# Kernel tuning notes

Hardware: AMD Instinct MI355X
Metric: run time of the kernel (lower is better)

## Reference

```python
import jax, jax.numpy as jnp
import numpy as np

N_NODES = 50000
N_EDGES = 800000
IN_DIM, H1, H2, OUT_DIM = 128, 512, 256, 1


def glorot(key, shape):
    fan_in, fan_out = shape
    lim = jnp.sqrt(6.0 / (fan_in + fan_out))
    return jax.random.uniform(key, shape, jnp.float32, -lim, lim)


def setup_inputs() -> dict:
    key = jax.random.key(0)
    ks = jax.random.split(key, 6)
    x = jax.random.normal(ks[0], (N_NODES, IN_DIM), jnp.float32)
    edge_index = jax.random.randint(ks[1], (2, N_EDGES), 0, N_NODES, jnp.int32)
    edge_attr = jax.random.uniform(ks[2], (N_EDGES,), jnp.float32)
    return {
        "x": x,
        "edge_index": edge_index,
        "edge_attr": edge_attr,
        "W1": glorot(ks[3], (IN_DIM, H1)), "b1": jnp.zeros((H1,), jnp.float32),
        "W2": glorot(ks[4], (H1, H2)), "b2": jnp.zeros((H2,), jnp.float32),
        "W3": glorot(ks[5], (H2, OUT_DIM)), "b3": jnp.zeros((OUT_DIM,), jnp.float32),
    }


def gcn_conv(x, src, dst, ew, W, b, n_nodes):
    # PyG GCNConv with edge weights, normalize=True, add_self_loops=True.
    h = x @ W                                            # [N, F_out]
    # degree includes self-loop weight 1.0 at each node
    deg = jax.ops.segment_sum(ew, dst, num_segments=n_nodes) + 1.0  # [N]
    dis = jnp.where(deg > 0, jax.lax.rsqrt(deg), 0.0)    # deg^{-1/2}
    norm = dis[src] * ew * dis[dst]                      # [E]
    msgs = h[src] * norm[:, None]                        # [E, F_out] gather
    agg = jax.ops.segment_sum(msgs, dst, num_segments=n_nodes)      # scatter-add
    # self-loop contribution: norm_ii = dis_i * 1 * dis_i = 1/deg_i
    agg = agg + h * (dis * dis)[:, None]
    return agg + b


def reference(x, edge_index, edge_attr, W1, b1, W2, b2, W3, b3):
    src, dst = edge_index[0], edge_index[1]
    n = x.shape[0]
    h = jax.nn.relu(gcn_conv(x, src, dst, edge_attr, W1, b1, n))
    h = jax.nn.relu(gcn_conv(h, src, dst, edge_attr, W2, b2, n))
    return gcn_conv(h, src, dst, edge_attr, W3, b3, n)
```

## Files before the change

kernel.cpp:

```cpp
#include <hip/hip_runtime.h>
#include <hip/hip_bf16.h>
#include <stdint.h>

typedef unsigned short u16;
typedef unsigned long long u64;
typedef __attribute__((ext_vector_type(8))) short bf16x8;
typedef __attribute__((ext_vector_type(4))) float f32x4;

constexpr int N_NODES = 50000;
constexpr int N_EDGES = 800000;
constexpr int IN_DIM  = 128;
constexpr int H1_DIM  = 512;
constexpr int H2_DIM  = 256;
constexpr int MT      = 64;
constexpr int MP      = 50048;

constexpr float DEG_SCALE = 268435456.0f;
constexpr float DEG_INV   = 1.0f / 268435456.0f;

__device__ __forceinline__ u16 f2b(float f) {
  union { float f; unsigned u; } v{f};
  unsigned r = v.u + 0x7fff + ((v.u >> 16) & 1);
  return (u16)(r >> 16);
}
__device__ __forceinline__ float b2f(u16 h) {
  union { unsigned u; float f; } v;
  v.u = ((unsigned)h) << 16;
  return v.f;
}

__device__ __forceinline__ void async16(void* lds, const void* g) {
  __builtin_amdgcn_global_load_lds(
      (const __attribute__((address_space(1))) unsigned int*)g,
      (__attribute__((address_space(3))) unsigned int*)lds, 16, 0, 0);
}

__global__ __launch_bounds__(256) void deg_hist_kernel(
    const int* __restrict__ dst, const float* __restrict__ ew,
    u64* __restrict__ degcnt, int E) {
  int e = blockIdx.x * 256 + threadIdx.x;
  if (e >= E) return;
  int d = dst[e];
  u64 inc = ((u64)1 << 40) | (u64)(ew[e] * DEG_SCALE + 0.5f);
  atomicAdd(&degcnt[d], inc);
}

__global__ __launch_bounds__(256) void scan1_kernel(
    const u64* __restrict__ degcnt, int* __restrict__ counts,
    float* __restrict__ dis, int* __restrict__ row_ptr,
    int* __restrict__ bsum, int n) {
  __shared__ int ws[4];
  int b = blockIdx.x, t = threadIdx.x, idx = b * 256 + t;
  int lane = t & 63, wid = t >> 6;
  u64 v = (idx < n) ? degcnt[idx] : 0;
  int cnt = (int)(v >> 40);
  if (idx < n) {
    counts[idx] = cnt;
    float deg = (float)(v & 0xFFFFFFFFFFULL) * DEG_INV;
    dis[idx] = rsqrtf(deg + 1.0f);
  }
  int val = cnt;
#pragma unroll
  for (int off = 1; off < 64; off <<= 1) {
    int u = __shfl_up(val, off);
    if (lane >= off) val += u;
  }
  if (lane == 63) ws[wid] = val;
  __syncthreads();
  if (t == 0) {
    int s = 0;
#pragma unroll
    for (int j = 0; j < 4; ++j) { int q = ws[j]; ws[j] = s; s += q; }
    bsum[b] = s;
  }
  __syncthreads();
  val += ws[wid];
  if (idx < n) row_ptr[idx + 1] = val;
}

__global__ __launch_bounds__(256) void scan2_kernel(int* bsum, int nb) {
  __shared__ int ws[4];
  int t = threadIdx.x;
  int lane = t & 63, wid = t >> 6;
  int self = (t < nb) ? bsum[t] : 0;
  int val = self;
#pragma unroll
  for (int off = 1; off < 64; off <<= 1) {
    int u = __shfl_up(val, off);
    if (lane >= off) val += u;
  }
  if (lane == 63) ws[wid] = val;
  __syncthreads();
  if (t == 0) {
    int s = 0;
#pragma unroll
    for (int j = 0; j < 4; ++j) { int q = ws[j]; ws[j] = s; s += q; }
  }
  __syncthreads();
  val += ws[wid];
  if (t < nb) bsum[t] = val - self;
}

__global__ __launch_bounds__(256) void scan3_kernel(
    int* __restrict__ row_ptr, const int* __restrict__ bsum, int n) {
  int idx = blockIdx.x * 256 + threadIdx.x;
  if (idx < n) row_ptr[idx + 1] += bsum[blockIdx.x];
  if (idx == 0) row_ptr[0] = 0;
}

__global__ __launch_bounds__(256) void fill_kernel(
    const int* __restrict__ src, const int* __restrict__ dst,
    const float* __restrict__ ew, const float* __restrict__ dis,
    const int* __restrict__ row_ptr, int* __restrict__ counts,
    u64* __restrict__ erec, int E) {
  int e = blockIdx.x * 256 + threadIdx.x;
  if (e >= E) return;
  int d = dst[e], s = src[e];
  int pos = row_ptr[d] + atomicSub(&counts[d], 1) - 1;
  float nm = dis[s] * ew[e] * dis[d];
  erec[pos] = ((u64)__float_as_uint(nm) << 32) | (unsigned)s;
}

__global__ __launch_bounds__(256) void cvt_bf16_kernel(
    const float* __restrict__ in, u16* __restrict__ out, int n4) {
  int i = blockIdx.x * 256 + threadIdx.x;
  if (i >= n4) return;
  float4 v = *(const float4*)&in[(size_t)i * 4];
  ushort4 o;
  o.x = f2b(v.x); o.y = f2b(v.y); o.z = f2b(v.z); o.w = f2b(v.w);
  *(ushort4*)&out[(size_t)i * 4] = o;
}

__global__ __launch_bounds__(256) void agg128_kernel(
    const u16* __restrict__ X, const int* __restrict__ row_ptr,
    const u64* __restrict__ erec, const float* __restrict__ dis,
    u16* __restrict__ Y, int n) {
  int wid = threadIdx.x >> 6, lane = threadIdx.x & 63;
  int node = blockIdx.x * 4 + wid;
  if (node >= n) return;
  float d = dis[node];
  float dd = d * d;
  const u16* Xl = X + lane * 2;
  ushort2 sv = *(const ushort2*)(Xl + (size_t)node * 128);
  float a0 = b2f(sv.x) * dd, a1 = b2f(sv.y) * dd;
  int e0 = row_ptr[node], e1 = row_ptr[node + 1];
  for (int base = e0; base < e1; base += 64) {
    int cnt = min(64, e1 - base);
    u64 rec = 0;
    if (lane < cnt) rec = erec[base + lane];
    int sl = (int)(unsigned)rec;
    float wl = __uint_as_float((unsigned)(rec >> 32));
    int j = 0;
    for (; j + 4 <= cnt; j += 4) {
      int   s0 = __shfl(sl, j),     s1 = __shfl(sl, j + 1);
      int   s2 = __shfl(sl, j + 2), s3 = __shfl(sl, j + 3);
      float w0 = __shfl(wl, j),     w1 = __shfl(wl, j + 1);
      float w2 = __shfl(wl, j + 2), w3 = __shfl(wl, j + 3);
      ushort2 v0 = *(const ushort2*)(Xl + (size_t)s0 * 128);
      ushort2 v1 = *(const ushort2*)(Xl + (size_t)s1 * 128);
      ushort2 v2 = *(const ushort2*)(Xl + (size_t)s2 * 128);
      ushort2 v3 = *(const ushort2*)(Xl + (size_t)s3 * 128);
      a0 += b2f(v0.x) * w0; a1 += b2f(v0.y) * w0;
      a0 += b2f(v1.x) * w1; a1 += b2f(v1.y) * w1;
      a0 += b2f(v2.x) * w2; a1 += b2f(v2.y) * w2;
      a0 += b2f(v3.x) * w3; a1 += b2f(v3.y) * w3;
    }
    for (; j < cnt; ++j) {
      int s0 = __shfl(sl, j); float w0 = __shfl(wl, j);
      ushort2 v0 = *(const ushort2*)(Xl + (size_t)s0 * 128);
      a0 += b2f(v0.x) * w0; a1 += b2f(v0.y) * w0;
    }
  }
  unsigned pk = ((unsigned)f2b(a1) << 16) | (unsigned)f2b(a0);
  *(unsigned*)(Y + (size_t)node * 128 + lane * 2) = pk;
}

__global__ __launch_bounds__(256) void agg256_gemv_kernel(
    const u16* __restrict__ X, const int* __restrict__ row_ptr,
    const u64* __restrict__ erec, const float* __restrict__ dis,
    const float* __restrict__ b2, const float* __restrict__ W3,
    float* __restrict__ T, int n) {
  int wid = threadIdx.x >> 6, lane = threadIdx.x & 63;
  int node = blockIdx.x * 4 + wid;
  if (node >= n) return;
  float d = dis[node];
  float dd = d * d;
  const u16* Xl = X + lane * 4;
  ushort4 sv = *(const ushort4*)(Xl + (size_t)node * 256);
  float a0 = b2f(sv.x) * dd, a1 = b2f(sv.y) * dd;
  float a2 = b2f(sv.z) * dd, a3 = b2f(sv.w) * dd;
  int e0 = row_ptr[node], e1 = row_ptr[node + 1];
  for (int base = e0; base < e1; base += 64) {
    int cnt = min(64, e1 - base);
    u64 rec = 0;
    if (lane < cnt) rec = erec[base + lane];
    int sl = (int)(unsigned)rec;
    float wl = __uint_as_float((unsigned)(rec >> 32));
    int j = 0;
    for (; j + 4 <= cnt; j += 4) {
      int   s0 = __shfl(sl, j),     s1 = __shfl(sl, j + 1);
      int   s2 = __shfl(sl, j + 2), s3 = __shfl(sl, j + 3);
      float w0 = __shfl(wl, j),     w1 = __shfl(wl, j + 1);
      float w2 = __shfl(wl, j + 2), w3 = __shfl(wl, j + 3);
      ushort4 v0 = *(const ushort4*)(Xl + (size_t)s0 * 256);
      ushort4 v1 = *(const ushort4*)(Xl + (size_t)s1 * 256);
      ushort4 v2 = *(const ushort4*)(Xl + (size_t)s2 * 256);
      ushort4 v3 = *(const ushort4*)(Xl + (size_t)s3 * 256);
      a0 += b2f(v0.x) * w0; a1 += b2f(v0.y) * w0;
      a2 += b2f(v0.z) * w0; a3 += b2f(v0.w) * w0;
      a0 += b2f(v1.x) * w1; a1 += b2f(v1.y) * w1;
      a2 += b2f(v1.z) * w1; a3 += b2f(v1.w) * w1;
      a0 += b2f(v2.x) * w2; a1 += b2f(v2.y) * w2;
      a2 += b2f(v2.z) * w2; a3 += b2f(v2.w) * w2;
      a0 += b2f(v3.x) * w3; a1 += b2f(v3.y) * w3;
      a2 += b2f(v3.z) * w3; a3 += b2f(v3.w) * w3;
    }
    for (; j < cnt; ++j) {
      int s0 = __shfl(sl, j); float w0 = __shfl(wl, j);
      ushort4 v0 = *(const ushort4*)(Xl + (size_t)s0 * 256);
      a0 += b2f(v0.x) * w0; a1 += b2f(v0.y) * w0;
      a2 += b2f(v0.z) * w0; a3 += b2f(v0.w) * w0;
    }
  }
  float4 bv = *(const float4*)&b2[lane * 4];
  float4 wv = *(const float4*)&W3[lane * 4];
  float s = fmaxf(a0 + bv.x, 0.f) * wv.x + fmaxf(a1 + bv.y, 0.f) * wv.y +
            fmaxf(a2 + bv.z, 0.f) * wv.z + fmaxf(a3 + bv.w, 0.f) * wv.w;
#pragma unroll
  for (int off = 32; off; off >>= 1) s += __shfl_down(s, off);
  if (lane == 0) T[node] = s;
}

__global__ __launch_bounds__(256) void transpose_bf16_kernel(
    const float* __restrict__ W, u16* __restrict__ Wt, int K, int N) {
  int i = blockIdx.x * 256 + threadIdx.x;
  if (i >= N * K) return;
  int n = i / K, k = i - n * K;
  Wt[i] = f2b(W[(size_t)k * N + n]);
}

__global__ __launch_bounds__(512, 4) void fused_gemm_kernel(
    const u16* __restrict__ xa, const u16* __restrict__ w1t,
    const u16* __restrict__ w2t, const float* __restrict__ b1,
    u16* __restrict__ t2b, int Mstore) {
  __shared__ u16 xa_s[MT * 128];
  __shared__ u16 h1_s[MT * 128];
  __shared__ u16 ws_s[256 * 64];
  int tid = threadIdx.x;
  int m0 = blockIdx.x * MT;
  int lane = tid & 63, w = tid >> 6;
  int l15 = lane & 15, l4 = lane >> 4;
  int wa = w >> 1;
  int wb = w & 1;

  {
    const char* xb = (const char*)xa + (size_t)m0 * 256;
#pragma unroll
    for (int i = 0; i < 2; ++i) {
      int L = i * 8192 + tid * 16;
      int row = L >> 8;
      int srcoff = (row << 8) + ((L & 255) ^ ((row & 7) << 4));
      async16((char*)xa_s + i * 8192 + (tid & ~63) * 16, xb + srcoff);
    }
  }

  f32x4 acc2[4][2];
#pragma unroll
  for (int i = 0; i < 4; ++i)
#pragma unroll
    for (int j = 0; j < 2; ++j) acc2[i][j] = (f32x4){0.f, 0.f, 0.f, 0.f};

  for (int c = 0; c < 4; ++c) {
    f32x4 acc1[2][2];
#pragma unroll
    for (int i = 0; i < 2; ++i)
#pragma unroll
      for (int j = 0; j < 2; ++j) acc1[i][j] = (f32x4){0.f, 0.f, 0.f, 0.f};

#pragma unroll
    for (int ko = 0; ko < 2; ++ko) {
      {
        const char* wsrc = (const char*)w1t + (size_t)(c * 128) * 256 + ko * 128;
#pragma unroll
        for (int i = 0; i < 2; ++i) {
          int L = i * 8192 + tid * 16;
          int row = L >> 7;
          int srcoff = (row << 8) + ((L & 127) ^ ((row & 7) << 4));
          async16((char*)ws_s + i * 8192 + (tid & ~63) * 16, wsrc + srcoff);
        }
      }
      __syncthreads();
#pragma unroll
      for (int ki = 0; ki < 2; ++ki) {
        bf16x8 a1[2], bx[2];
#pragma unroll
        for (int fn = 0; fn < 2; ++fn) {
          int nr = wa * 32 + fn * 16 + l15;
          int byte = (nr * 128 + ki * 64 + l4 * 16) ^ ((nr & 7) << 4);
          a1[fn] = *(const bf16x8*)((const char*)ws_s + byte);
        }
#pragma unroll
        for (int fm = 0; fm < 2; ++fm) {
          int mr = wb * 32 + fm * 16 + l15;
          int byte = (mr * 256 + ko * 128 + ki * 64 + l4 * 16) ^ ((mr & 7) << 4);
          bx[fm] = *(const bf16x8*)((const char*)xa_s + byte);
        }
#pragma unroll
        for (int fn = 0; fn < 2; ++fn)
#pragma unroll
          for (int fm = 0; fm < 2; ++fm)
            acc1[fn][fm] = __builtin_amdgcn_mfma_f32_16x16x32_bf16(
                a1[fn], bx[fm], acc1[fn][fm], 0, 0, 0);
      }
      __syncthreads();
    }

#pragma unroll
    for (int fn = 0; fn < 2; ++fn) {
      int nloc = wa * 32 + fn * 16 + l4 * 4;
      float4 bv = *(const float4*)&b1[c * 128 + nloc];
#pragma unroll
      for (int fm = 0; fm < 2; ++fm) {
        int mr = wb * 32 + fm * 16 + l15;
        u16 p0 = f2b(fmaxf(acc1[fn][fm][0] + bv.x, 0.f));
        u16 p1 = f2b(fmaxf(acc1[fn][fm][1] + bv.y, 0.f));
        u16 p2 = f2b(fmaxf(acc1[fn][fm][2] + bv.z, 0.f));
        u16 p3 = f2b(fmaxf(acc1[fn][fm][3] + bv.w, 0.f));
        u64 pk = ((u64)p3 << 48) | ((u64)p2 << 32) | ((u64)p1 << 16) | p0;
        int byte = (mr * 256 + nloc * 2) ^ ((mr & 7) << 4);
        *(u64*)((char*)h1_s + byte) = pk;
      }
    }
    __syncthreads();

#pragma unroll
    for (int ko = 0; ko < 2; ++ko) {
      {
        const char* wsrc = (const char*)w2t + (size_t)(c * 128 + ko * 64) * 2;
#pragma unroll
        for (int i = 0; i < 4; ++i) {
          int L = i * 8192 + tid * 16;
          int row = L >> 7;
          int srcoff = row * 1024 + ((L & 127) ^ ((row & 7) << 4));
          async16((char*)ws_s + i * 8192 + (tid & ~63) * 16, wsrc + srcoff);
        }
      }
      __syncthreads();
#pragma unroll
      for (int ki = 0; ki < 2; ++ki) {
        bf16x8 a2[4], bh[2];
#pragma unroll
        for (int fnn = 0; fnn < 4; ++fnn) {
          int nr = wa * 64 + fnn * 16 + l15;
          int byte = (nr * 128 + ki * 64 + l4 * 16) ^ ((nr & 7) << 4);
          a2[fnn] = *(const bf16x8*)((const char*)ws_s + byte);
        }
#pragma unroll
        for (int fm = 0; fm < 2; ++fm) {
          int mr = wb * 32 + fm * 16 + l15;
          int byte = (mr * 256 + ko * 128 + ki * 64 + l4 * 16) ^ ((mr & 7) << 4);
          bh[fm] = *(const bf16x8*)((const char*)h1_s + byte);
        }
#pragma unroll
        for (int fnn = 0; fnn < 4; ++fnn)
#pragma unroll
          for (int fm = 0; fm < 2; ++fm)
            acc2[fnn][fm] = __builtin_amdgcn_mfma_f32_16x16x32_bf16(
                a2[fnn], bh[fm], acc2[fnn][fm], 0, 0, 0);
      }
      __syncthreads();
    }
  }

#pragma unroll
  for (int fnn = 0; fnn < 4; ++fnn) {
    int nn = wa * 64 + fnn * 16 + l4 * 4;
#pragma unroll
    for (int fm = 0; fm < 2; ++fm) {
      int m = m0 + wb * 32 + fm * 16 + l15;
      if (m < Mstore) {
        ushort4 pk;
        pk.x = f2b(acc2[fnn][fm][0]);
        pk.y = f2b(acc2[fnn][fm][1]);
        pk.z = f2b(acc2[fnn][fm][2]);
        pk.w = f2b(acc2[fnn][fm][3]);
        *(ushort4*)(t2b + (size_t)m * 256 + nn) = pk;
      }
    }
  }
}

__global__ __launch_bounds__(256) void agg_out_kernel(
    const float* __restrict__ T, const int* __restrict__ row_ptr,
    const u64* __restrict__ erec, const float* __restrict__ dis,
    const float* __restrict__ b3, float* __restrict__ out, int n) {
  const int2* E2 = (const int2*)erec;
  int i = blockIdx.x * 256 + threadIdx.x;
  if (i >= n) return;
  float d = dis[i];
  float acc = T[i] * d * d;
  int e = row_ptr[i], e1 = row_ptr[i + 1];
  for (; e + 4 <= e1; e += 4) {
    int2 q0 = E2[e], q1 = E2[e + 1], q2 = E2[e + 2], q3 = E2[e + 3];
    acc += T[q0.x] * __int_as_float(q0.y) + T[q1.x] * __int_as_float(q1.y) +
           T[q2.x] * __int_as_float(q2.y) + T[q3.x] * __int_as_float(q3.y);
  }
  for (; e < e1; ++e) {
    int2 q = E2[e];
    acc += T[q.x] * __int_as_float(q.y);
  }
  out[i] = acc + b3[0];
}

extern "C" void kernel_launch(void* const* d_in, const int* in_sizes, int n_in,
                              void* d_out, int out_size, void* d_ws, size_t ws_size,
                              hipStream_t stream) {
  const float* x  = (const float*)d_in[0];
  const int*   ei = (const int*)d_in[1];
  const float* ew = (const float*)d_in[2];
  const float* W1 = (const float*)d_in[3];
  const float* b1 = (const float*)d_in[4];
  const float* W2 = (const float*)d_in[5];
  const float* b2 = (const float*)d_in[6];
  const float* W3 = (const float*)d_in[7];
  const float* b3 = (const float*)d_in[8];
  float* out = (float*)d_out;

  const int N = N_NODES, E = N_EDGES;
  const int* src = ei;
  const int* dst = ei + E;
  const int NB = (N + 255) / 256;

  char* p = (char*)d_ws;
  auto alloc = [&](size_t bytes) -> char* {
    char* r = p;
    p += (bytes + 255) & ~(size_t)255;
    return r;
  };
  u64*   degcnt  = (u64*)  alloc((size_t)N * 8);
  float* dis     = (float*)alloc((size_t)N * 4);
  int*   row_ptr = (int*)  alloc((size_t)(N + 1) * 4);
  int*   counts  = (int*)  alloc((size_t)N * 4);
  int*   bsum    = (int*)  alloc((size_t)NB * 4);
  u64*   erec    = (u64*)  alloc((size_t)E * 8);
  u16*   w1t     = (u16*)  alloc((size_t)H1_DIM * IN_DIM * 2);
  u16*   w2t     = (u16*)  alloc((size_t)H2_DIM * H1_DIM * 2);
  u16*   xb      = (u16*)  alloc((size_t)N * IN_DIM * 2);
  u16*   xa      = (u16*)  alloc((size_t)MP * IN_DIM * 2);
  u16*   t2b     = (u16*)  alloc((size_t)N * H2_DIM * 2);
  float* t3      = (float*)alloc((size_t)N * 4);

  transpose_bf16_kernel<<<(H1_DIM * IN_DIM + 255) / 256, 256, 0, stream>>>(
      W1, w1t, IN_DIM, H1_DIM);
  transpose_bf16_kernel<<<(H2_DIM * H1_DIM + 255) / 256, 256, 0, stream>>>(
      W2, w2t, H1_DIM, H2_DIM);
  cvt_bf16_kernel<<<(N * IN_DIM / 4 + 255) / 256, 256, 0, stream>>>(
      x, xb, N * IN_DIM / 4);

  hipMemsetAsync(degcnt, 0, (size_t)N * 8, stream);
  deg_hist_kernel<<<(E + 255) / 256, 256, 0, stream>>>(dst, ew, degcnt, E);

  scan1_kernel<<<NB, 256, 0, stream>>>(degcnt, counts, dis, row_ptr, bsum, N);
  scan2_kernel<<<1, 256, 0, stream>>>(bsum, NB);
  scan3_kernel<<<NB, 256, 0, stream>>>(row_ptr, bsum, N);
  fill_kernel<<<(E + 255) / 256, 256, 0, stream>>>(src, dst, ew, dis, row_ptr,
                                                   counts, erec, E);

  hipMemsetAsync(xa + (size_t)N * IN_DIM, 0, (size_t)(MP - N) * IN_DIM * 2, stream);

  agg128_kernel<<<(N + 3) / 4, 256, 0, stream>>>(xb, row_ptr, erec, dis, xa, N);

  fused_gemm_kernel<<<MP / MT, 512, 0, stream>>>(xa, w1t, w2t, b1, t2b, N);

  agg256_gemv_kernel<<<(N + 3) / 4, 256, 0, stream>>>(
      t2b, row_ptr, erec, dis, b2, W3, t3, N);

  agg_out_kernel<<<(N + 255) / 256, 256, 0, stream>>>(t3, row_ptr, erec, dis,
                                                      b3, out, N);
}
```

Before: 240.5 us.

## Pad CSR rows to multiples of 8 and merge prep kernels into one launch

Rounds each node's CSR row length up to a multiple of 8, with zero-filled padding records (weight 0, source 0). The gather loops in all three aggregation kernels can then run fixed 8-wide unrolled batches without tail loops or bounds checks, and the scalar output kernel reads records as int4 pairs. It also folds the degree histogram, x-to-bf16 conversion and both weight transposes into one prep kernel, saving launches. The cost is a larger edge buffer that must be memset each call, plus wasted gathers on padded slots.

```diff
diff --git a/kernel.cpp b/kernel.cpp
--- a/kernel.cpp
+++ b/kernel.cpp
@@ -14,6 +14,8 @@
 constexpr int H2_DIM  = 256;
 constexpr int MT      = 64;
 constexpr int MP      = 50048;
+constexpr int EPAD    = N_EDGES + 7 * N_NODES + 64;
+constexpr int PREP_NB = 3125;
 
 constexpr float DEG_SCALE = 268435456.0f;
 constexpr float DEG_INV   = 1.0f / 268435456.0f;
@@ -35,14 +37,41 @@
       (__attribute__((address_space(3))) unsigned int*)lds, 16, 0, 0);
 }
 
-__global__ __launch_bounds__(256) void deg_hist_kernel(
+__global__ __launch_bounds__(256) void prep_kernel(
     const int* __restrict__ dst, const float* __restrict__ ew,
-    u64* __restrict__ degcnt, int E) {
-  int e = blockIdx.x * 256 + threadIdx.x;
-  if (e >= E) return;
-  int d = dst[e];
-  u64 inc = ((u64)1 << 40) | (u64)(ew[e] * DEG_SCALE + 0.5f);
-  atomicAdd(&degcnt[d], inc);
+    u64* __restrict__ degcnt,
+    const float* __restrict__ x, u16* __restrict__ xb,
+    const float* __restrict__ W1, u16* __restrict__ w1t,
+    const float* __restrict__ W2, u16* __restrict__ w2t) {
+  int b = blockIdx.x, t = threadIdx.x;
+  {
+    int e = b * 256 + t;
+    int d = dst[e];
+    u64 inc = ((u64)1 << 40) | (u64)(ew[e] * DEG_SCALE + 0.5f);
+    atomicAdd(&degcnt[d], inc);
+  }
+#pragma unroll
+  for (int r = 0; r < 2; ++r) {
+    int i = b * 512 + r * 256 + t;
+    float4 v = *(const float4*)&x[(size_t)i * 4];
+    ushort4 o;
+    o.x = f2b(v.x); o.y = f2b(v.y); o.z = f2b(v.z); o.w = f2b(v.w);
+    *(ushort4*)&xb[(size_t)i * 4] = o;
+  }
+  if (t < 21) {
+    int i = b * 21 + t;
+    if (i < H1_DIM * IN_DIM) {
+      int nn = i / IN_DIM, k = i - nn * IN_DIM;
+      w1t[i] = f2b(W1[(size_t)k * H1_DIM + nn]);
+    }
+  }
+  if (t < 42) {
+    int i = b * 42 + t;
+    if (i < H2_DIM * H1_DIM) {
+      int nn = i / H1_DIM, k = i - nn * H1_DIM;
+      w2t[i] = f2b(W2[(size_t)k * H2_DIM + nn]);
+    }
+  }
 }
 
 __global__ __launch_bounds__(256) void scan1_kernel(
@@ -59,7 +88,7 @@
     float deg = (float)(v & 0xFFFFFFFFFFULL) * DEG_INV;
     dis[idx] = rsqrtf(deg + 1.0f);
   }
-  int val = cnt;
+  int val = (cnt + 7) & ~7;
 #pragma unroll
   for (int off = 1; off < 64; off <<= 1) {
     int u = __shfl_up(val, off);
@@ -119,16 +148,6 @@
   int pos = row_ptr[d] + atomicSub(&counts[d], 1) - 1;
   float nm = dis[s] * ew[e] * dis[d];
   erec[pos] = ((u64)__float_as_uint(nm) << 32) | (unsigned)s;
-}
-
-__global__ __launch_bounds__(256) void cvt_bf16_kernel(
-    const float* __restrict__ in, u16* __restrict__ out, int n4) {
-  int i = blockIdx.x * 256 + threadIdx.x;
-  if (i >= n4) return;
-  float4 v = *(const float4*)&in[(size_t)i * 4];
-  ushort4 o;
-  o.x = f2b(v.x); o.y = f2b(v.y); o.z = f2b(v.z); o.w = f2b(v.w);
-  *(ushort4*)&out[(size_t)i * 4] = o;
 }
 
 __global__ __launch_bounds__(256) void agg128_kernel(
@@ -146,29 +165,24 @@
   int e0 = row_ptr[node], e1 = row_ptr[node + 1];
   for (int base = e0; base < e1; base += 64) {
     int cnt = min(64, e1 - base);
-    u64 rec = 0;
-    if (lane < cnt) rec = erec[base + lane];
+    u64 rec = erec[base + lane];
     int sl = (int)(unsigned)rec;
     float wl = __uint_as_float((unsigned)(rec >> 32));
-    int j = 0;
-    for (; j + 4 <= cnt; j += 4) {
-      int   s0 = __shfl(sl, j),     s1 = __shfl(sl, j + 1);
-      int   s2 = __shfl(sl, j + 2), s3 = __shfl(sl, j + 3);
-      float w0 = __shfl(wl, j),     w1 = __shfl(wl, j + 1);
-      float w2 = __shfl(wl, j + 2), w3 = __shfl(wl, j + 3);
-      ushort2 v0 = *(const ushort2*)(Xl + (size_t)s0 * 128);
-      ushort2 v1 = *(const ushort2*)(Xl + (size_t)s1 * 128);
-      ushort2 v2 = *(const ushort2*)(Xl + (size_t)s2 * 128);
-      ushort2 v3 = *(const ushort2*)(Xl + (size_t)s3 * 128);
-      a0 += b2f(v0.x) * w0; a1 += b2f(v0.y) * w0;
-      a0 += b2f(v1.x) * w1; a1 += b2f(v1.y) * w1;
-      a0 += b2f(v2.x) * w2; a1 += b2f(v2.y) * w2;
-      a0 += b2f(v3.x) * w3; a1 += b2f(v3.y) * w3;
-    }
-    for (; j < cnt; ++j) {
-      int s0 = __shfl(sl, j); float w0 = __shfl(wl, j);
-      ushort2 v0 = *(const ushort2*)(Xl + (size_t)s0 * 128);
-      a0 += b2f(v0.x) * w0; a1 += b2f(v0.y) * w0;
+    for (int j = 0; j < cnt; j += 8) {
+      int ss[8]; float ww[8]; ushort2 vv[8];
+#pragma unroll
+      for (int q = 0; q < 8; ++q) {
+        ss[q] = __shfl(sl, j + q);
+        ww[q] = __shfl(wl, j + q);
+      }
+#pragma unroll
+      for (int q = 0; q < 8; ++q)
+        vv[q] = *(const ushort2*)(Xl + (size_t)ss[q] * 128);
+#pragma unroll
+      for (int q = 0; q < 8; ++q) {
+        a0 += b2f(vv[q].x) * ww[q];
+        a1 += b2f(vv[q].y) * ww[q];
+      }
     }
   }
   unsigned pk = ((unsigned)f2b(a1) << 16) | (unsigned)f2b(a0);
@@ -192,34 +206,26 @@
   int e0 = row_ptr[node], e1 = row_ptr[node + 1];
   for (int base = e0; base < e1; base += 64) {
     int cnt = min(64, e1 - base);
-    u64 rec = 0;
-    if (lane < cnt) rec = erec[base + lane];
+    u64 rec = erec[base + lane];
     int sl = (int)(unsigned)rec;
     float wl = __uint_as_float((unsigned)(rec >> 32));
-    int j = 0;
-    for (; j + 4 <= cnt; j += 4) {
-      int   s0 = __shfl(sl, j),     s1 = __shfl(sl, j + 1);
-      int   s2 = __shfl(sl, j + 2), s3 = __shfl(sl, j + 3);
-      float w0 = __shfl(wl, j),     w1 = __shfl(wl, j + 1);
-      float w2 = __shfl(wl, j + 2), w3 = __shfl(wl, j + 3);
-      ushort4 v0 = *(const ushort4*)(Xl + (size_t)s0 * 256);
-      ushort4 v1 = *(const ushort4*)(Xl + (size_t)s1 * 256);
-      ushort4 v2 = *(const ushort4*)(Xl + (size_t)s2 * 256);
-      ushort4 v3 = *(const ushort4*)(Xl + (size_t)s3 * 256);
-      a0 += b2f(v0.x) * w0; a1 += b2f(v0.y) * w0;
-      a2 += b2f(v0.z) * w0; a3 += b2f(v0.w) * w0;
-      a0 += b2f(v1.x) * w1; a1 += b2f(v1.y) * w1;
-      a2 += b2f(v1.z) * w1; a3 += b2f(v1.w) * w1;
-      a0 += b2f(v2.x) * w2; a1 += b2f(v2.y) * w2;
-      a2 += b2f(v2.z) * w2; a3 += b2f(v2.w) * w2;
-      a0 += b2f(v3.x) * w3; a1 += b2f(v3.y) * w3;
-      a2 += b2f(v3.z) * w3; a3 += b2f(v3.w) * w3;
-    }
-    for (; j < cnt; ++j) {
-      int s0 = __shfl(sl, j); float w0 = __shfl(wl, j);
-      ushort4 v0 = *(const ushort4*)(Xl + (size_t)s0 * 256);
-      a0 += b2f(v0.x) * w0; a1 += b2f(v0.y) * w0;
-      a2 += b2f(v0.z) * w0; a3 += b2f(v0.w) * w0;
+    for (int j = 0; j < cnt; j += 8) {
+      int ss[8]; float ww[8]; ushort4 vv[8];
+#pragma unroll
+      for (int q = 0; q < 8; ++q) {
+        ss[q] = __shfl(sl, j + q);
+        ww[q] = __shfl(wl, j + q);
+      }
+#pragma unroll
+      for (int q = 0; q < 8; ++q)
+        vv[q] = *(const ushort4*)(Xl + (size_t)ss[q] * 256);
+#pragma unroll
+      for (int q = 0; q < 8; ++q) {
+        a0 += b2f(vv[q].x) * ww[q];
+        a1 += b2f(vv[q].y) * ww[q];
+        a2 += b2f(vv[q].z) * ww[q];
+        a3 += b2f(vv[q].w) * ww[q];
+      }
     }
   }
   float4 bv = *(const float4*)&b2[lane * 4];
@@ -229,14 +235,6 @@
 #pragma unroll
   for (int off = 32; off; off >>= 1) s += __shfl_down(s, off);
   if (lane == 0) T[node] = s;
-}
-
-__global__ __launch_bounds__(256) void transpose_bf16_kernel(
-    const float* __restrict__ W, u16* __restrict__ Wt, int K, int N) {
-  int i = blockIdx.x * 256 + threadIdx.x;
-  if (i >= N * K) return;
-  int n = i / K, k = i - n * K;
-  Wt[i] = f2b(W[(size_t)k * N + n]);
 }
 
 __global__ __launch_bounds__(512, 4) void fused_gemm_kernel(
@@ -394,20 +392,19 @@
     const float* __restrict__ T, const int* __restrict__ row_ptr,
     const u64* __restrict__ erec, const float* __restrict__ dis,
     const float* __restrict__ b3, float* __restrict__ out, int n) {
-  const int2* E2 = (const int2*)erec;
+  const int4* E4 = (const int4*)erec;
   int i = blockIdx.x * 256 + threadIdx.x;
   if (i >= n) return;
   float d = dis[i];
   float acc = T[i] * d * d;
-  int e = row_ptr[i], e1 = row_ptr[i + 1];
-  for (; e + 4 <= e1; e += 4) {
-    int2 q0 = E2[e], q1 = E2[e + 1], q2 = E2[e + 2], q3 = E2[e + 3];
-    acc += T[q0.x] * __int_as_float(q0.y) + T[q1.x] * __int_as_float(q1.y) +
-           T[q2.x] * __int_as_float(q2.y) + T[q3.x] * __int_as_float(q3.y);
-  }
-  for (; e < e1; ++e) {
-    int2 q = E2[e];
-    acc += T[q.x] * __int_as_float(q.y);
+  int e0 = row_ptr[i], e1 = row_ptr[i + 1];
+  for (int e = e0; e < e1; e += 8) {
+    int h = e >> 1;
+    int4 r0 = E4[h], r1 = E4[h + 1], r2 = E4[h + 2], r3 = E4[h + 3];
+    acc += T[r0.x] * __int_as_float(r0.y) + T[r0.z] * __int_as_float(r0.w) +
+           T[r1.x] * __int_as_float(r1.y) + T[r1.z] * __int_as_float(r1.w) +
+           T[r2.x] * __int_as_float(r2.y) + T[r2.z] * __int_as_float(r2.w) +
+           T[r3.x] * __int_as_float(r3.y) + T[r3.z] * __int_as_float(r3.w);
   }
   out[i] = acc + b3[0];
 }
@@ -442,7 +439,7 @@
   int*   row_ptr = (int*)  alloc((size_t)(N + 1) * 4);
   int*   counts  = (int*)  alloc((size_t)N * 4);
   int*   bsum    = (int*)  alloc((size_t)NB * 4);
-  u64*   erec    = (u64*)  alloc((size_t)E * 8);
+  u64*   erec    = (u64*)  alloc((size_t)EPAD * 8);
   u16*   w1t     = (u16*)  alloc((size_t)H1_DIM * IN_DIM * 2);
   u16*   w2t     = (u16*)  alloc((size_t)H2_DIM * H1_DIM * 2);
   u16*   xb      = (u16*)  alloc((size_t)N * IN_DIM * 2);
@@ -450,15 +447,12 @@
   u16*   t2b     = (u16*)  alloc((size_t)N * H2_DIM * 2);
   float* t3      = (float*)alloc((size_t)N * 4);
 
-  transpose_bf16_kernel<<<(H1_DIM * IN_DIM + 255) / 256, 256, 0, stream>>>(
-      W1, w1t, IN_DIM, H1_DIM);
-  transpose_bf16_kernel<<<(H2_DIM * H1_DIM + 255) / 256, 256, 0, stream>>>(
-      W2, w2t, H1_DIM, H2_DIM);
-  cvt_bf16_kernel<<<(N * IN_DIM / 4 + 255) / 256, 256, 0, stream>>>(
-      x, xb, N * IN_DIM / 4);
-
   hipMemsetAsync(degcnt, 0, (size_t)N * 8, stream);
-  deg_hist_kernel<<<(E + 255) / 256, 256, 0, stream>>>(dst, ew, degcnt, E);
+  hipMemsetAsync(erec, 0, (size_t)EPAD * 8, stream);
+  hipMemsetAsync(xa + (size_t)N * IN_DIM, 0, (size_t)(MP - N) * IN_DIM * 2, stream);
+
+  prep_kernel<<<PREP_NB, 256, 0, stream>>>(dst, ew, degcnt, x, xb,
+                                           W1, w1t, W2, w2t);
 
   scan1_kernel<<<NB, 256, 0, stream>>>(degcnt, counts, dis, row_ptr, bsum, N);
   scan2_kernel<<<1, 256, 0, stream>>>(bsum, NB);
@@ -466,8 +460,6 @@
   fill_kernel<<<(E + 255) / 256, 256, 0, stream>>>(src, dst, ew, dis, row_ptr,
                                                    counts, erec, E);
 
-  hipMemsetAsync(xa + (size_t)N * IN_DIM, 0, (size_t)(MP - N) * IN_DIM * 2, stream);
-
   agg128_kernel<<<(N + 3) / 4, 256, 0, stream>>>(xb, row_ptr, erec, dis, xa, N);
 
   fused_gemm_kernel<<<MP / MT, 512, 0, stream>>>(xa, w1t, w2t, b1, t2b, N);
```

Measured after the change: 233.3 us. 3.0% less time.
